# Kernel tuning notes

Measured on AMD Instinct MI355X. Metric: run time of the kernel, lower is better.

The kernel has to match this reference:

```python
import jax, jax.numpy as jnp
import numpy as np

N_NODES = 50000


def gcn_conv_max(x, edge_index, edge_weight, W, b):
    """PyG GCNConv with aggr='max': gcn_norm (add self-loops, symmetric
    degree normalization), linear transform, gather-scale-scatter_max, bias."""
    n = x.shape[0]
    row, col = edge_index[0], edge_index[1]
    loop = jnp.arange(n)
    row = jnp.concatenate([row, loop])  # sources (incl. self-loops)
    col = jnp.concatenate([col, loop])  # targets
    ew = jnp.concatenate([edge_weight, jnp.ones((n,), x.dtype)])
    deg = jax.ops.segment_sum(ew, col, num_segments=n)
    dis = jnp.where(deg > 0, jax.lax.rsqrt(deg), jnp.zeros_like(deg))
    norm = dis[row] * ew * dis[col]  # [E+N]
    h = x @ W                         # [N, out]
    msg = norm[:, None] * h[row]      # gather + scale, [E+N, out]
    agg = jax.ops.segment_max(msg, col, num_segments=n)  # scatter-max
    return agg + b


def setup_inputs() -> dict:
    key = jax.random.key(0)
    ks = jax.random.split(key, 9)
    N, E = N_NODES, 1_600_000
    x = jax.random.normal(ks[0], (N, 5), dtype=jnp.float32)
    edge_index = jax.random.randint(ks[1], (2, E), 0, N, dtype=jnp.int64)
    edge_weight = jax.random.uniform(ks[2], (E,), dtype=jnp.float32)
    s1 = 1.0 / np.sqrt(5.0)
    s2 = 1.0 / np.sqrt(240.0)
    W1 = jax.random.uniform(ks[3], (5, 240), jnp.float32, -s1, s1)
    b1 = jnp.zeros((240,), jnp.float32)
    W2 = jax.random.uniform(ks[4], (240, 240), jnp.float32, -s2, s2)
    b2 = jnp.zeros((240,), jnp.float32)
    We = jax.random.uniform(ks[5], (240, 80), jnp.float32, -s2, s2)
    be = jnp.zeros((80,), jnp.float32)
    return {"x": x, "edge_index": edge_index, "edge_weight": edge_weight,
            "W1": W1, "b1": b1, "W2": W2, "b2": b2, "We": We, "be": be}


def reference(x, edge_index, edge_weight, W1, b1, W2, b2, We, be):
    h = gcn_conv_max(x, edge_index, edge_weight, W1, b1)
    h = jax.nn.relu(h)
    h = gcn_conv_max(h, edge_index, edge_weight, W2, b2)
    h = jax.nn.relu(h)
    return h @ We + be  # [N, 80]
```

## Files before the change

kernel.cpp:

```cpp
#include <hip/hip_runtime.h>
#include <cfloat>

#define HID 240

static inline size_t alignUp(size_t x, size_t a){ return (x + a - 1) / a * a; }

typedef __bf16 bf16x8 __attribute__((ext_vector_type(8)));
typedef unsigned short u16x8 __attribute__((ext_vector_type(8)));
typedef float  f32x16 __attribute__((ext_vector_type(16)));

__device__ __forceinline__ float b2f(unsigned short u){
    return __uint_as_float(((unsigned)u) << 16);
}
__device__ __forceinline__ unsigned short f2b_rne(float f){
    unsigned r = __float_as_uint(f);
    r += 0x7FFFu + ((r >> 16) & 1u);
    return (unsigned short)(r >> 16);
}

__global__ void k_deg_hist(const int* __restrict__ col, const float* __restrict__ ew,
                           unsigned long long* __restrict__ pk,
                           unsigned* __restrict__ rank, int E){
    int e = blockIdx.x * blockDim.x + threadIdx.x;
    if (e < E){
        int c = col[e];
        unsigned q = __float2uint_rn(ew[e] * 1048576.0f);
        unsigned long long old = atomicAdd(&pk[c], (1ull << 40) | (unsigned long long)q);
        rank[e] = (unsigned)(old >> 40);
    }
}

__global__ void k_dis_prep(const unsigned long long* __restrict__ pk,
                           float* __restrict__ dis, unsigned* __restrict__ cnt,
                           unsigned* __restrict__ bsum, int N, int nb,
                           const float* __restrict__ x, float* __restrict__ xp,
                           const float* __restrict__ W1, unsigned short* __restrict__ W1f,
                           const float* __restrict__ W2, unsigned short* __restrict__ Bt2h,
                           unsigned short* __restrict__ Bt2l,
                           const float* __restrict__ We, unsigned short* __restrict__ Bt3h,
                           unsigned short* __restrict__ Bt3l){
    int b = blockIdx.x;
    int t = threadIdx.x;
    if (b < nb){
        int i = b * 256 + t;
        unsigned v = 0u;
        if (i < N){
            unsigned long long p = pk[i];
            unsigned c = (unsigned)(p >> 40);
            cnt[i] = c;
            float deg = 1.0f + (float)(p & 0xFFFFFFFFFFull) * (1.0f / 1048576.0f);
            dis[i] = rsqrtf(deg);
            v = (c + 32u) >> 5;
        }
        #pragma unroll
        for (int o = 32; o > 0; o >>= 1) v += __shfl_down(v, (unsigned)o, 64);
        __shared__ unsigned ws[4];
        int lane = t & 63, w = t >> 6;
        if (lane == 0) ws[w] = v;
        __syncthreads();
        if (t == 0) bsum[b] = ws[0] + ws[1] + ws[2] + ws[3];
        return;
    }
    int bb = b - nb;
    if (bb < nb){
        __shared__ float s[1280];
        int rbase = bb * 256;
        #pragma unroll
        for (int c = 0; c < 5; c++){
            int idx = rbase * 5 + t + 256 * c;
            s[t + 256 * c] = (idx < N * 5) ? x[idx] : 0.0f;
        }
        __syncthreads();
        #pragma unroll
        for (int c = 0; c < 8; c++){
            int pos = t + 256 * c;
            int r = pos >> 3, j = pos & 7;
            int grow = rbase + r;
            if (grow < N)
                xp[(size_t)grow * 8 + j] = (j < 5) ? s[r * 5 + j] : 0.0f;
        }
        return;
    }
    bb -= nb;
    if (bb < 32){
        int i = bb * 256 + t;
        if (i < 2 * 8 * 64 * 8){
            int k    = i & 7;
            int lane = (i >> 3) & 63;
            int j    = (i >> 9) & 7;
            int s2   = i >> 12;
            int lm = lane & 31, quad = lane >> 5;
            int kg = quad * 8 + k;
            int colm = 32 * j + lm;
            float v = (kg < 5 && colm < HID) ? W1[kg * HID + colm] : 0.0f;
            unsigned short hi = f2b_rne(v);
            W1f[i] = (s2 == 0) ? hi : f2b_rne(v - b2f(hi));
        }
        return;
    }
    bb -= 32;
    if (bb < 240){
        int i = bb * 256 + t;
        int n = i / HID, k = i - n * HID;
        float v = (n < HID) ? W2[(size_t)k * HID + n] : 0.0f;
        unsigned short hi = f2b_rne(v);
        Bt2h[i] = hi;
        Bt2l[i] = f2b_rne(v - b2f(hi));
        return;
    }
    bb -= 240;
    {
        int i = bb * 256 + t;
        if (i < 128 * HID){
            int n = i / HID, k = i - n * HID;
            float v = (n < 80) ? We[(size_t)k * 80 + n] : 0.0f;
            unsigned short hi = f2b_rne(v);
            Bt3h[i] = hi;
            Bt3l[i] = f2b_rne(v - b2f(hi));
        }
    }
}

__global__ void k_bscan(const unsigned* __restrict__ bsum, unsigned* __restrict__ boff,
                        unsigned* __restrict__ poff, int nb, int N){
    __shared__ unsigned s[256];
    int t = threadIdx.x;
    unsigned v = (t < nb) ? bsum[t] : 0u;
    s[t] = v;
    __syncthreads();
    for (int o = 1; o < 256; o <<= 1){
        unsigned u = (t >= o) ? s[t - o] : 0u;
        __syncthreads();
        s[t] += u;
        __syncthreads();
    }
    if (t < nb) boff[t] = s[t] - v;
    if (t == 0) poff[N] = 32u * s[nb - 1];
}

__global__ void k_offs_fill(const unsigned* __restrict__ cnt, const unsigned* __restrict__ boff,
                            const float* __restrict__ dis,
                            unsigned* __restrict__ poff, int2* __restrict__ sedge, int N){
    int b = blockIdx.x, t = threadIdx.x;
    int i = b * 256 + t;
    unsigned c = (i < N) ? cnt[i] : 0u;
    unsigned v = (i < N) ? ((c + 32u) >> 5) : 0u;
    int lane = t & 63, w = t >> 6;
    unsigned x = v;
    #pragma unroll
    for (int o = 1; o < 64; o <<= 1){
        unsigned u = __shfl_up(x, (unsigned)o, 64);
        if (lane >= o) x += u;
    }
    __shared__ unsigned ws[4];
    if (lane == 63) ws[w] = x;
    __syncthreads();
    unsigned wb = 0;
    if (w > 0) wb += ws[0];
    if (w > 1) wb += ws[1];
    if (w > 2) wb += ws[2];
    if (i < N){
        unsigned p = 32u * (boff[b] + wb + x - v);
        poff[i] = p;
        float dd = dis[i];
        int2 sv = make_int2(i, __float_as_int(dd * dd));
        sedge[p] = sv;
        unsigned s1 = p + 32u * v;
        for (unsigned s = p + 1u + c; s < s1; s++) sedge[s] = sv;
    }
}

__global__ void k_scatter(const int* __restrict__ row, const int* __restrict__ col,
                          const float* __restrict__ ew, const float* __restrict__ dis,
                          const unsigned* __restrict__ poff, const unsigned* __restrict__ rank,
                          int2* __restrict__ sedge, int E){
    int e = blockIdx.x * blockDim.x + threadIdx.x;
    if (e < E){
        int r = row[e], c = col[e];
        float nw = dis[r] * ew[e] * dis[c];
        unsigned p = poff[c] + 1u + rank[e];
        sedge[p] = make_int2(r, __float_as_int(nw));
    }
}

__global__ __launch_bounds__(256) void k_agg1m(const float* __restrict__ xp,
                                               const unsigned short* __restrict__ W1f,
                                               const unsigned* __restrict__ cnt,
                                               const unsigned* __restrict__ poff,
                                               const int2* __restrict__ sedge,
                                               const float* __restrict__ bias,
                                               float* __restrict__ out, int N, int nwaves){
    int wid  = blockIdx.x * 4 + (threadIdx.x >> 6);
    int lane = threadIdx.x & 63;
    int lm   = lane & 31;

    bf16x8 bh[8], bl[8];
    #pragma unroll
    for (int j = 0; j < 8; j++){
        bh[j] = *(const bf16x8*)(W1f + ((size_t)(0 * 8 + j) * 64 + lane) * 8);
        bl[j] = *(const bf16x8*)(W1f + ((size_t)(1 * 8 + j) * 64 + lane) * 8);
    }
    float bv[8];
    #pragma unroll
    for (int j = 0; j < 8; j++){
        int c = 32 * j + lm;
        bv[j] = (c < HID) ? bias[c] : 0.0f;
    }
    const f32x16 zv = {};

    for (int d = wid; d < N; d += nwaves){
        unsigned base = poff[d];
        unsigned nch  = (cnt[d] + 32u) >> 5;
        float m[8];
        #pragma unroll
        for (int j = 0; j < 8; j++) m[j] = -FLT_MAX;

        for (unsigned c = 0; c < nch; c++){
            u16x8 ahu = (u16x8)0, alu = (u16x8)0;
            if (lane < 32){
                int2 e = sedge[base + 32u * c + (unsigned)lm];
                float w = __int_as_float(e.y);
                const float4* xr = (const float4*)(xp + (size_t)e.x * 8);
                float4 x0 = xr[0], x1 = xr[1];
                float p[5] = {w * x0.x, w * x0.y, w * x0.z, w * x0.w, w * x1.x};
                #pragma unroll
                for (int k = 0; k < 5; k++){
                    unsigned short h = f2b_rne(p[k]);
                    ahu[k] = h;
                    alu[k] = f2b_rne(p[k] - b2f(h));
                }
            }
            bf16x8 ah = __builtin_bit_cast(bf16x8, ahu);
            bf16x8 al = __builtin_bit_cast(bf16x8, alu);
            #pragma unroll
            for (int j = 0; j < 8; j += 2){
                f32x16 a0 = __builtin_amdgcn_mfma_f32_32x32x16_bf16(ah, bh[j],     zv, 0, 0, 0);
                f32x16 a1 = __builtin_amdgcn_mfma_f32_32x32x16_bf16(ah, bh[j + 1], zv, 0, 0, 0);
                a0 = __builtin_amdgcn_mfma_f32_32x32x16_bf16(ah, bl[j],     a0, 0, 0, 0);
                a1 = __builtin_amdgcn_mfma_f32_32x32x16_bf16(ah, bl[j + 1], a1, 0, 0, 0);
                a0 = __builtin_amdgcn_mfma_f32_32x32x16_bf16(al, bh[j],     a0, 0, 0, 0);
                a1 = __builtin_amdgcn_mfma_f32_32x32x16_bf16(al, bh[j + 1], a1, 0, 0, 0);
                #pragma unroll
                for (int r = 0; r < 16; r++){
                    m[j]     = fmaxf(m[j],     a0[r]);
                    m[j + 1] = fmaxf(m[j + 1], a1[r]);
                }
            }
        }
        float o[8];
        #pragma unroll
        for (int j = 0; j < 8; j++){
            float other = __shfl_xor(m[j], 32, 64);
            o[j] = fmaxf(fmaxf(m[j], other) + bv[j], 0.0f);
        }
        if (lane < 32){
            float* orow = out + (size_t)d * HID;
            #pragma unroll
            for (int j = 0; j < 8; j++){
                int c = 32 * j + lm;
                if (c < HID) orow[c] = o[j];
            }
        }
    }
}

template <bool OB16>
__global__ __launch_bounds__(256) void k_gemm_mfma(const float* __restrict__ A,
                                                   const unsigned short* __restrict__ Bth,
                                                   const unsigned short* __restrict__ Btl,
                                                   const float* __restrict__ bias,
                                                   void* __restrict__ Cv,
                                                   int M, int Ncol, int Npad){
    __shared__ unsigned short As_hi[32][24];
    __shared__ unsigned short As_lo[32][24];
    const int K = 240;
    int t = threadIdx.x;
    int wave = t >> 6, lane = t & 63;
    int m0 = blockIdx.x * 32;
    int n0 = wave * 64;
    bool wact = n0 < Npad;

    int lm   = lane & 31;
    int quad = lane >> 5;

    f32x16 acc0 = {};
    f32x16 acc1 = {};

    for (int k0 = 0; k0 < K; k0 += 16){
        if (t < 128){
            int m = t >> 2, kq = (t & 3) * 4;
            float4 av = make_float4(0.f, 0.f, 0.f, 0.f);
            if (m0 + m < M) av = *(const float4*)(A + (size_t)(m0 + m) * K + k0 + kq);
            ushort4 hi, lo;
            hi.x = f2b_rne(av.x); lo.x = f2b_rne(av.x - b2f(hi.x));
            hi.y = f2b_rne(av.y); lo.y = f2b_rne(av.y - b2f(hi.y));
            hi.z = f2b_rne(av.z); lo.z = f2b_rne(av.z - b2f(hi.z));
            hi.w = f2b_rne(av.w); lo.w = f2b_rne(av.w - b2f(hi.w));
            *(ushort4*)&As_hi[m][kq] = hi;
            *(ushort4*)&As_lo[m][kq] = lo;
        }
        __syncthreads();
        if (wact){
            bf16x8 ah = *(const bf16x8*)&As_hi[lm][quad * 8];
            bf16x8 al = *(const bf16x8*)&As_lo[lm][quad * 8];
            size_t bo0 = (size_t)(n0 + lm) * K + k0 + quad * 8;
            size_t bo1 = (size_t)(n0 + 32 + lm) * K + k0 + quad * 8;
            bf16x8 bh0 = *(const bf16x8*)(Bth + bo0);
            bf16x8 bl0 = *(const bf16x8*)(Btl + bo0);
            bf16x8 bh1 = *(const bf16x8*)(Bth + bo1);
            bf16x8 bl1 = *(const bf16x8*)(Btl + bo1);
            acc0 = __builtin_amdgcn_mfma_f32_32x32x16_bf16(ah, bh0, acc0, 0, 0, 0);
            acc0 = __builtin_amdgcn_mfma_f32_32x32x16_bf16(ah, bl0, acc0, 0, 0, 0);
            acc0 = __builtin_amdgcn_mfma_f32_32x32x16_bf16(al, bh0, acc0, 0, 0, 0);
            acc1 = __builtin_amdgcn_mfma_f32_32x32x16_bf16(ah, bh1, acc1, 0, 0, 0);
            acc1 = __builtin_amdgcn_mfma_f32_32x32x16_bf16(ah, bl1, acc1, 0, 0, 0);
            acc1 = __builtin_amdgcn_mfma_f32_32x32x16_bf16(al, bh1, acc1, 0, 0, 0);
        }
        __syncthreads();
    }

    if (!wact) return;
    #pragma unroll
    for (int h = 0; h < 2; h++){
        int n = n0 + 32 * h + lm;
        if (n >= Ncol) continue;
        float bvv = (!OB16 && bias) ? bias[n] : 0.0f;
        #pragma unroll
        for (int r = 0; r < 16; r++){
            int m = m0 + (r & 3) + 8 * (r >> 2) + 4 * quad;
            if (m >= M) continue;
            float v = (h == 0) ? acc0[r] : acc1[r];
            if (OB16){
                ((unsigned short*)Cv)[(size_t)m * Ncol + n] = f2b_rne(v);
            } else {
                ((float*)Cv)[(size_t)m * Ncol + n] = v + bvv;
            }
        }
    }
}

__global__ __launch_bounds__(256) void k_aggb(const unsigned short* __restrict__ H2,
                                              const unsigned* __restrict__ cnt,
                                              const unsigned* __restrict__ poff,
                                              const int2* __restrict__ sedge,
                                              const float* __restrict__ bias,
                                              float* __restrict__ out, int N){
    int d    = blockIdx.x * 4 + (threadIdx.x >> 6);
    int lane = threadIdx.x & 63;
    if (d >= N) return;
    bool act = lane < 60;

    float4 m = make_float4(-FLT_MAX, -FLT_MAX, -FLT_MAX, -FLT_MAX);
    unsigned p0 = poff[d], p1 = p0 + 1u + cnt[d];
    unsigned p = p0;
    for (; p + 4 <= p1; p += 4){
        int2 e0 = sedge[p], e1 = sedge[p+1], e2 = sedge[p+2], e3 = sedge[p+3];
        if (act){
            ushort4 g0 = ((const ushort4*)(H2 + (size_t)e0.x * HID))[lane];
            ushort4 g1 = ((const ushort4*)(H2 + (size_t)e1.x * HID))[lane];
            ushort4 g2 = ((const ushort4*)(H2 + (size_t)e2.x * HID))[lane];
            ushort4 g3 = ((const ushort4*)(H2 + (size_t)e3.x * HID))[lane];
            float w0 = __int_as_float(e0.y), w1 = __int_as_float(e1.y);
            float w2 = __int_as_float(e2.y), w3 = __int_as_float(e3.y);
            m.x = fmaxf(fmaxf(m.x, w0*b2f(g0.x)), fmaxf(w1*b2f(g1.x), fmaxf(w2*b2f(g2.x), w3*b2f(g3.x))));
            m.y = fmaxf(fmaxf(m.y, w0*b2f(g0.y)), fmaxf(w1*b2f(g1.y), fmaxf(w2*b2f(g2.y), w3*b2f(g3.y))));
            m.z = fmaxf(fmaxf(m.z, w0*b2f(g0.z)), fmaxf(w1*b2f(g1.z), fmaxf(w2*b2f(g2.z), w3*b2f(g3.z))));
            m.w = fmaxf(fmaxf(m.w, w0*b2f(g0.w)), fmaxf(w1*b2f(g1.w), fmaxf(w2*b2f(g2.w), w3*b2f(g3.w))));
        }
    }
    for (; p < p1; p++){
        int2 e0 = sedge[p];
        if (act){
            ushort4 g0 = ((const ushort4*)(H2 + (size_t)e0.x * HID))[lane];
            float w0 = __int_as_float(e0.y);
            m.x = fmaxf(m.x, w0 * b2f(g0.x)); m.y = fmaxf(m.y, w0 * b2f(g0.y));
            m.z = fmaxf(m.z, w0 * b2f(g0.z)); m.w = fmaxf(m.w, w0 * b2f(g0.w));
        }
    }
    if (act){
        float4 b = ((const float4*)bias)[lane];
        float4 o;
        o.x = fmaxf(m.x + b.x, 0.0f);
        o.y = fmaxf(m.y + b.y, 0.0f);
        o.z = fmaxf(m.z + b.z, 0.0f);
        o.w = fmaxf(m.w + b.w, 0.0f);
        ((float4*)(out + (size_t)d * HID))[lane] = o;
    }
}

extern "C" void kernel_launch(void* const* d_in, const int* in_sizes, int n_in,
                              void* d_out, int out_size, void* d_ws, size_t ws_size,
                              hipStream_t stream){
    const float* x  = (const float*)d_in[0];
    const int*   ei = (const int*)  d_in[1];
    const float* ew = (const float*)d_in[2];
    const float* W1 = (const float*)d_in[3];
    const float* b1 = (const float*)d_in[4];
    const float* W2 = (const float*)d_in[5];
    const float* b2 = (const float*)d_in[6];
    const float* We = (const float*)d_in[7];
    const float* be = (const float*)d_in[8];
    float* out = (float*)d_out;

    const int N = in_sizes[0] / 5;
    const int E = in_sizes[2];
    const int* row = ei;
    const int* col = ei + E;
    const int nb = (N + 255) / 256;

    char* w = (char*)d_ws;
    size_t o = 0;
    auto alloc = [&](size_t bytes) -> void* {
        void* p = w + o;
        o = alignUp(o + bytes, 256);
        return p;
    };
    unsigned long long* pk = (unsigned long long*) alloc((size_t)N * 8);
    float*          dis   = (float*)          alloc((size_t)N * 4);
    unsigned*       cnt   = (unsigned*)       alloc((size_t)N * 4);
    unsigned*       poff  = (unsigned*)       alloc((size_t)(N + 1) * 4);
    unsigned*       bsum  = (unsigned*)       alloc((size_t)nb * 4);
    unsigned*       boff  = (unsigned*)       alloc((size_t)nb * 4);
    unsigned*       rank  = (unsigned*)       alloc((size_t)E * 4);
    int2*           sedge = (int2*)           alloc(((size_t)E + 32u * N + 64u) * 8);
    float*          xp    = (float*)          alloc((size_t)N * 8 * 4);
    unsigned short* W1f   = (unsigned short*) alloc((size_t)2 * 8 * 64 * 8 * 2);
    unsigned short* Bt2h  = (unsigned short*) alloc((size_t)256 * HID * 2);
    unsigned short* Bt2l  = (unsigned short*) alloc((size_t)256 * HID * 2);
    unsigned short* Bt3h  = (unsigned short*) alloc((size_t)128 * HID * 2);
    unsigned short* Bt3l  = (unsigned short*) alloc((size_t)128 * HID * 2);
    unsigned short* bufH2 = (unsigned short*) alloc((size_t)N * HID * 2);
    float*          bufB  = (float*)          alloc((size_t)N * HID * 4);
    (void)ws_size; (void)n_in; (void)out_size;

    int be_ = (E + 255) / 256;

    hipMemsetAsync(pk, 0, (size_t)N * 8, stream);
    k_deg_hist <<<be_, 256, 0, stream>>>(col, ew, pk, rank, E);
    k_dis_prep <<<nb + nb + 32 + 240 + 120, 256, 0, stream>>>(pk, dis, cnt, bsum, N, nb,
                                                              x, xp, W1, W1f,
                                                              W2, Bt2h, Bt2l,
                                                              We, Bt3h, Bt3l);
    k_bscan    <<<1, 256, 0, stream>>>(bsum, boff, poff, nb, N);
    k_offs_fill<<<nb, 256, 0, stream>>>(cnt, boff, dis, poff, sedge, N);
    k_scatter  <<<be_, 256, 0, stream>>>(row, col, ew, dis, poff, rank, sedge, E);

    const int a1blocks = 1536;
    k_agg1m<<<a1blocks, 256, 0, stream>>>(xp, W1f, cnt, poff, sedge, b1, bufB, N, a1blocks * 4);

    int gm = (N + 31) / 32;
    k_gemm_mfma<true><<<gm, 256, 0, stream>>>(bufB, Bt2h, Bt2l, nullptr, bufH2, N, HID, 256);
    k_aggb<<<(N + 3) / 4, 256, 0, stream>>>(bufH2, cnt, poff, sedge, b2, bufB, N);

    k_gemm_mfma<false><<<gm, 256, 0, stream>>>(bufB, Bt3h, Bt3l, be, out, N, 80, 128);
}
```

Before: 512.4 us.

## Enlarge GEMM M-tile to 64 rows and fold degree histogram into prep kernel

The MFMA GEMM now covers 64 rows per block instead of 32. Each wave keeps a 2x2 set of accumulators, so every B-fragment load from global memory feeds twice as many MFMAs and the grid is half as large. Separately, the edge degree-histogram atomics are merged into the weight/feature prep kernel as extra blocks, and the dis/bsum computation is moved into a new small kernel. This restructures the launch sequence without changing the kernel count. The cost is more accumulator registers per wave, which may reduce occupancy, and fewer GEMM blocks to spread across CUs.

Measured after the change: 497.2 us. 1.03x faster.

```diff
diff --git a/kernel.cpp b/kernel.cpp
--- a/kernel.cpp
+++ b/kernel.cpp
@@ -18,21 +18,9 @@
     return (unsigned short)(r >> 16);
 }
 
-__global__ void k_deg_hist(const int* __restrict__ col, const float* __restrict__ ew,
-                           unsigned long long* __restrict__ pk,
-                           unsigned* __restrict__ rank, int E){
-    int e = blockIdx.x * blockDim.x + threadIdx.x;
-    if (e < E){
-        int c = col[e];
-        unsigned q = __float2uint_rn(ew[e] * 1048576.0f);
-        unsigned long long old = atomicAdd(&pk[c], (1ull << 40) | (unsigned long long)q);
-        rank[e] = (unsigned)(old >> 40);
-    }
-}
-
-__global__ void k_dis_prep(const unsigned long long* __restrict__ pk,
-                           float* __restrict__ dis, unsigned* __restrict__ cnt,
-                           unsigned* __restrict__ bsum, int N, int nb,
+__global__ void k_deg_prep(const int* __restrict__ col, const float* __restrict__ ew,
+                           unsigned long long* __restrict__ pk, unsigned* __restrict__ rank,
+                           int E, int ne, int N, int nb,
                            const float* __restrict__ x, float* __restrict__ xp,
                            const float* __restrict__ W1, unsigned short* __restrict__ W1f,
                            const float* __restrict__ W2, unsigned short* __restrict__ Bt2h,
@@ -41,27 +29,17 @@
                            unsigned short* __restrict__ Bt3l){
     int b = blockIdx.x;
     int t = threadIdx.x;
-    if (b < nb){
-        int i = b * 256 + t;
-        unsigned v = 0u;
-        if (i < N){
-            unsigned long long p = pk[i];
-            unsigned c = (unsigned)(p >> 40);
-            cnt[i] = c;
-            float deg = 1.0f + (float)(p & 0xFFFFFFFFFFull) * (1.0f / 1048576.0f);
-            dis[i] = rsqrtf(deg);
-            v = (c + 32u) >> 5;
-        }
-        #pragma unroll
-        for (int o = 32; o > 0; o >>= 1) v += __shfl_down(v, (unsigned)o, 64);
-        __shared__ unsigned ws[4];
-        int lane = t & 63, w = t >> 6;
-        if (lane == 0) ws[w] = v;
-        __syncthreads();
-        if (t == 0) bsum[b] = ws[0] + ws[1] + ws[2] + ws[3];
+    if (b < ne){
+        int e = b * 256 + t;
+        if (e < E){
+            int c = col[e];
+            unsigned q = __float2uint_rn(ew[e] * 1048576.0f);
+            unsigned long long old = atomicAdd(&pk[c], (1ull << 40) | (unsigned long long)q);
+            rank[e] = (unsigned)(old >> 40);
+        }
         return;
     }
-    int bb = b - nb;
+    int bb = b - ne;
     if (bb < nb){
         __shared__ float s[1280];
         int rbase = bb * 256;
@@ -119,6 +97,29 @@
             Bt3l[i] = f2b_rne(v - b2f(hi));
         }
     }
+}
+
+__global__ void k_dis_bsum(const unsigned long long* __restrict__ pk,
+                           float* __restrict__ dis, unsigned* __restrict__ cnt,
+                           unsigned* __restrict__ bsum, int N){
+    int b = blockIdx.x;
+    int i = b * 256 + threadIdx.x;
+    unsigned v = 0u;
+    if (i < N){
+        unsigned long long p = pk[i];
+        unsigned c = (unsigned)(p >> 40);
+        cnt[i] = c;
+        float deg = 1.0f + (float)(p & 0xFFFFFFFFFFull) * (1.0f / 1048576.0f);
+        dis[i] = rsqrtf(deg);
+        v = (c + 32u) >> 5;
+    }
+    #pragma unroll
+    for (int o = 32; o > 0; o >>= 1) v += __shfl_down(v, (unsigned)o, 64);
+    __shared__ unsigned ws[4];
+    int lane = threadIdx.x & 63, w = threadIdx.x >> 6;
+    if (lane == 0) ws[w] = v;
+    __syncthreads();
+    if (threadIdx.x == 0) bsum[b] = ws[0] + ws[1] + ws[2] + ws[3];
 }
 
 __global__ void k_bscan(const unsigned* __restrict__ bsum, unsigned* __restrict__ boff,
@@ -271,23 +272,22 @@
                                                    const float* __restrict__ bias,
                                                    void* __restrict__ Cv,
                                                    int M, int Ncol, int Npad){
-    __shared__ unsigned short As_hi[32][24];
-    __shared__ unsigned short As_lo[32][24];
+    __shared__ unsigned short As_hi[64][24];
+    __shared__ unsigned short As_lo[64][24];
     const int K = 240;
     int t = threadIdx.x;
     int wave = t >> 6, lane = t & 63;
-    int m0 = blockIdx.x * 32;
+    int m0 = blockIdx.x * 64;
     int n0 = wave * 64;
     bool wact = n0 < Npad;
 
     int lm   = lane & 31;
     int quad = lane >> 5;
 
-    f32x16 acc0 = {};
-    f32x16 acc1 = {};
+    f32x16 acc[2][2] = {};
 
     for (int k0 = 0; k0 < K; k0 += 16){
-        if (t < 128){
+        {
             int m = t >> 2, kq = (t & 3) * 4;
             float4 av = make_float4(0.f, 0.f, 0.f, 0.f);
             if (m0 + m < M) av = *(const float4*)(A + (size_t)(m0 + m) * K + k0 + kq);
@@ -301,39 +301,45 @@
         }
         __syncthreads();
         if (wact){
-            bf16x8 ah = *(const bf16x8*)&As_hi[lm][quad * 8];
-            bf16x8 al = *(const bf16x8*)&As_lo[lm][quad * 8];
             size_t bo0 = (size_t)(n0 + lm) * K + k0 + quad * 8;
             size_t bo1 = (size_t)(n0 + 32 + lm) * K + k0 + quad * 8;
             bf16x8 bh0 = *(const bf16x8*)(Bth + bo0);
             bf16x8 bl0 = *(const bf16x8*)(Btl + bo0);
             bf16x8 bh1 = *(const bf16x8*)(Bth + bo1);
             bf16x8 bl1 = *(const bf16x8*)(Btl + bo1);
-            acc0 = __builtin_amdgcn_mfma_f32_32x32x16_bf16(ah, bh0, acc0, 0, 0, 0);
-            acc0 = __builtin_amdgcn_mfma_f32_32x32x16_bf16(ah, bl0, acc0, 0, 0, 0);
-            acc0 = __builtin_amdgcn_mfma_f32_32x32x16_bf16(al, bh0, acc0, 0, 0, 0);
-            acc1 = __builtin_amdgcn_mfma_f32_32x32x16_bf16(ah, bh1, acc1, 0, 0, 0);
-            acc1 = __builtin_amdgcn_mfma_f32_32x32x16_bf16(ah, bl1, acc1, 0, 0, 0);
-            acc1 = __builtin_amdgcn_mfma_f32_32x32x16_bf16(al, bh1, acc1, 0, 0, 0);
+            #pragma unroll
+            for (int mh = 0; mh < 2; mh++){
+                bf16x8 ah = *(const bf16x8*)&As_hi[32 * mh + lm][quad * 8];
+                bf16x8 al = *(const bf16x8*)&As_lo[32 * mh + lm][quad * 8];
+                acc[mh][0] = __builtin_amdgcn_mfma_f32_32x32x16_bf16(ah, bh0, acc[mh][0], 0, 0, 0);
+                acc[mh][0] = __builtin_amdgcn_mfma_f32_32x32x16_bf16(ah, bl0, acc[mh][0], 0, 0, 0);
+                acc[mh][0] = __builtin_amdgcn_mfma_f32_32x32x16_bf16(al, bh0, acc[mh][0], 0, 0, 0);
+                acc[mh][1] = __builtin_amdgcn_mfma_f32_32x32x16_bf16(ah, bh1, acc[mh][1], 0, 0, 0);
+                acc[mh][1] = __builtin_amdgcn_mfma_f32_32x32x16_bf16(ah, bl1, acc[mh][1], 0, 0, 0);
+                acc[mh][1] = __builtin_amdgcn_mfma_f32_32x32x16_bf16(al, bh1, acc[mh][1], 0, 0, 0);
+            }
         }
         __syncthreads();
     }
 
     if (!wact) return;
     #pragma unroll
-    for (int h = 0; h < 2; h++){
-        int n = n0 + 32 * h + lm;
-        if (n >= Ncol) continue;
-        float bvv = (!OB16 && bias) ? bias[n] : 0.0f;
+    for (int mh = 0; mh < 2; mh++){
         #pragma unroll
-        for (int r = 0; r < 16; r++){
-            int m = m0 + (r & 3) + 8 * (r >> 2) + 4 * quad;
-            if (m >= M) continue;
-            float v = (h == 0) ? acc0[r] : acc1[r];
-            if (OB16){
-                ((unsigned short*)Cv)[(size_t)m * Ncol + n] = f2b_rne(v);
-            } else {
-                ((float*)Cv)[(size_t)m * Ncol + n] = v + bvv;
+        for (int h = 0; h < 2; h++){
+            int n = n0 + 32 * h + lm;
+            if (n >= Ncol) continue;
+            float bvv = (!OB16 && bias) ? bias[n] : 0.0f;
+            #pragma unroll
+            for (int r = 0; r < 16; r++){
+                int m = m0 + 32 * mh + (r & 3) + 8 * (r >> 2) + 4 * quad;
+                if (m >= M) continue;
+                float v = acc[mh][h][r];
+                if (OB16){
+                    ((unsigned short*)Cv)[(size_t)m * Ncol + n] = f2b_rne(v);
+                } else {
+                    ((float*)Cv)[(size_t)m * Ncol + n] = v + bvv;
+                }
             }
         }
     }
@@ -433,22 +439,22 @@
     float*          bufB  = (float*)          alloc((size_t)N * HID * 4);
     (void)ws_size; (void)n_in; (void)out_size;
 
-    int be_ = (E + 255) / 256;
+    int ne = (E + 255) / 256;
 
     hipMemsetAsync(pk, 0, (size_t)N * 8, stream);
-    k_deg_hist <<<be_, 256, 0, stream>>>(col, ew, pk, rank, E);
-    k_dis_prep <<<nb + nb + 32 + 240 + 120, 256, 0, stream>>>(pk, dis, cnt, bsum, N, nb,
+    k_deg_prep <<<ne + nb + 32 + 240 + 120, 256, 0, stream>>>(col, ew, pk, rank, E, ne, N, nb,
                                                               x, xp, W1, W1f,
                                                               W2, Bt2h, Bt2l,
                                                               We, Bt3h, Bt3l);
+    k_dis_bsum <<<nb, 256, 0, stream>>>(pk, dis, cnt, bsum, N);
     k_bscan    <<<1, 256, 0, stream>>>(bsum, boff, poff, nb, N);
     k_offs_fill<<<nb, 256, 0, stream>>>(cnt, boff, dis, poff, sedge, N);
-    k_scatter  <<<be_, 256, 0, stream>>>(row, col, ew, dis, poff, rank, sedge, E);
+    k_scatter  <<<ne, 256, 0, stream>>>(row, col, ew, dis, poff, rank, sedge, E);
 
     const int a1blocks = 1536;
     k_agg1m<<<a1blocks, 256, 0, stream>>>(xp, W1f, cnt, poff, sedge, b1, bufB, N, a1blocks * 4);
 
-    int gm = (N + 31) / 32;
+    int gm = (N + 63) / 64;
     k_gemm_mfma<true><<<gm, 256, 0, stream>>>(bufB, Bt2h, Bt2l, nullptr, bufH2, N, HID, 256);
     k_aggb<<<(N + 3) / 4, 256, 0, stream>>>(bufH2, cnt, poff, sedge, b2, bufB, N);
 
```
